# Optimization experiments

Hardware: AMD Instinct MI355X
Metric: run time of the kernel (lower is better)

The kernel has to match this reference:

```python
import jax, jax.numpy as jnp
import numpy as np

NUM_USERS = 100000
NUM_ITEMS = 100000
EMB_DIM = 64
NUM_NODES = NUM_USERS + NUM_ITEMS
NUM_EDGES = 4000000
BATCH = 4096
NUM_LAYERS = 2


def setup_inputs() -> dict:
    key = jax.random.key(0)
    ks = jax.random.split(key, 8)
    user = jax.random.randint(ks[0], (BATCH,), 0, NUM_USERS, dtype=jnp.int64) if jax.config.jax_enable_x64 else jax.random.randint(ks[0], (BATCH,), 0, NUM_USERS, dtype=jnp.int32)
    pos = jax.random.randint(ks[1], (BATCH,), 0, NUM_ITEMS, dtype=jnp.int32)
    neg = jax.random.randint(ks[2], (BATCH,), 0, NUM_ITEMS, dtype=jnp.int32)
    edge_row = jax.random.randint(ks[3], (NUM_EDGES,), 0, NUM_NODES, dtype=jnp.int32)
    edge_col = jax.random.randint(ks[4], (NUM_EDGES,), 0, NUM_NODES, dtype=jnp.int32)
    # normalized adjacency values (degree-normalized in real LightGCN)
    edge_val = jax.random.uniform(ks[5], (NUM_EDGES,), dtype=jnp.float32) * 0.01
    user_emb = jax.random.normal(ks[6], (NUM_USERS, EMB_DIM), dtype=jnp.float32) * 0.01
    item_emb = jax.random.normal(ks[7], (NUM_ITEMS, EMB_DIM), dtype=jnp.float32) * 0.01
    return {"user": user, "pos": pos, "neg": neg,
            "edge_row": edge_row, "edge_col": edge_col, "edge_val": edge_val,
            "user_emb": user_emb, "item_emb": item_emb}


def _spmm(edge_row, edge_col, edge_val, x):
    # out[r] = sum_e val[e] * x[col[e]]  -- sparse adjacency times dense emb
    msgs = edge_val[:, None] * x[edge_col]  # [E, D]
    return jax.ops.segment_sum(msgs, edge_row, num_segments=NUM_NODES)


def reference(user, pos, neg, edge_row, edge_col, edge_val, user_emb, item_emb):
    all_emb = jnp.concatenate([user_emb, item_emb], axis=0)  # [N, D]
    acc = all_emb
    h = all_emb
    for _ in range(NUM_LAYERS):
        h = _spmm(edge_row, edge_col, edge_val, h)
        acc = acc + h
    lightgcn_out = acc / (NUM_LAYERS + 1)  # mean over stacked layer embeddings
    u = lightgcn_out[:NUM_USERS]
    i = lightgcn_out[NUM_USERS:]
    user_latent = u[user]          # [B, D]
    positive_latent = i[pos]       # [B, D]
    negative_latent = i[neg]       # [B, D]
    positive_score = jnp.sum(user_latent * positive_latent, axis=1)
    negative_score = jnp.sum(user_latent * negative_latent, axis=1)
    return positive_score, negative_score
```

## Files before the change

### kernel.cpp

```cpp
#include <hip/hip_runtime.h>
#include <cstdint>
#include <cstddef>

#define NUM_USERS 100000
#define NUM_ITEMS 100000
#define NUM_NODES 200000
#define NUM_EDGES 4000000
#define BATCH     4096
#define EMB       64

#define NB    391
#define CAP   11264
#define CHUNK 8192
#define PTHREADS 1024
#define EPB   8
#define RPT   11
#define NWORDS 6250


__device__ __forceinline__ unsigned short f2bf(float f) {
    unsigned u = __float_as_uint(f);
    u = (u + 0x7FFFu + ((u >> 16) & 1u)) >> 16;
    return (unsigned short)u;
}
__device__ __forceinline__ float bf2f(unsigned short b) {
    return __uint_as_float(((unsigned)b) << 16);
}


__global__ void k_part1(const int* __restrict__ user, const int* __restrict__ pos,
                        const int* __restrict__ neg,
                        const int* __restrict__ erow, const int* __restrict__ ecol,
                        const float* __restrict__ eval_,
                        const float* __restrict__ uemb, const float* __restrict__ iemb,
                        unsigned short* __restrict__ xb,
                        int* __restrict__ bcur,
                        unsigned* __restrict__ memb, unsigned* __restrict__ need,
                        int2* __restrict__ tmp) {
    __shared__ int  hist[NB];
    __shared__ int  sst[512];
    __shared__ int  gb[NB];
    __shared__ int2 srec[CHUNK];
    int t = threadIdx.x;
    int gid = blockIdx.x * PTHREADS + t;
    if (t < NB) hist[t] = 0;

    const int TOT8 = (NUM_NODES * EMB) / 8;
    const size_t UELEMS = (size_t)NUM_USERS * EMB;
    for (int i = gid; i < TOT8; i += gridDim.x * PTHREADS) {
        size_t off = (size_t)i * 8;
        const float* src = (off < UELEMS) ? (uemb + off) : (iemb + (off - UELEMS));
        float4 f0 = ((const float4*)src)[0];
        float4 f1 = ((const float4*)src)[1];
        ((ushort4*)(xb + off))[0] = make_ushort4(f2bf(f0.x), f2bf(f0.y), f2bf(f0.z), f2bf(f0.w));
        ((ushort4*)(xb + off))[1] = make_ushort4(f2bf(f1.x), f2bf(f1.y), f2bf(f1.z), f2bf(f1.w));
    }
    if (gid < 3 * BATCH) {
        int b = gid & (BATCH - 1);
        int w = gid >> 12;
        int node = (w == 0) ? user[b] : (w == 1) ? (NUM_USERS + pos[b]) : (NUM_USERS + neg[b]);
        unsigned bit = 1u << (node & 31);
        atomicOr(&memb[node >> 5], bit);
        atomicOr(&need[node >> 5], bit);
    }
    __syncthreads();

    int start = blockIdx.x * CHUNK;
    int rows[EPB], ranks[EPB];
#pragma unroll
    for (int k = 0; k < EPB; ++k) {
        int e = start + t + k * PTHREADS;
        if (e < NUM_EDGES) {
            int r = erow[e];
            rows[k]  = r;
            ranks[k] = atomicAdd(&hist[r >> 9], 1);
        } else {
            rows[k] = -1;
        }
    }
    __syncthreads();

    if (t < 512) sst[t] = (t < NB) ? hist[t] : 0;
    __syncthreads();
    for (int off = 1; off < 512; off <<= 1) {
        int add = 0;
        if (t < 512 && t >= off) add = sst[t - off];
        __syncthreads();
        if (t < 512 && t >= off) sst[t] += add;
        __syncthreads();
    }
    if (t < NB) gb[t] = atomicAdd(&bcur[t], hist[t]);

#pragma unroll
    for (int k = 0; k < EPB; ++k) {
        if (rows[k] >= 0) {
            int e   = start + t + k * PTHREADS;
            int r   = rows[k];
            int bkt = r >> 9;
            int lp  = sst[bkt] - hist[bkt] + ranks[k];
            srec[lp] = make_int2(((r & 511) << 18) | ecol[e], __float_as_int(eval_[e]));
        }
    }
    __syncthreads();

    int wv = t >> 6, ln = t & 63;
    for (int bkt = wv; bkt < NB; bkt += 16) {
        int c  = hist[bkt];
        int st = sst[bkt] - c;
        int g0 = gb[bkt];
        size_t base = (size_t)bkt * CAP;
        for (int j = ln; j < c; j += 64) {
            int rel = g0 + j;
            if (rel < CAP)
                tmp[base + rel] = srec[st + j];
        }
    }
}


__global__ void k_part2(const int* __restrict__ bcur, const int2* __restrict__ tmp,
                        const unsigned* __restrict__ memb,
                        int2* __restrict__ epack, int2* __restrict__ rowext,
                        unsigned* __restrict__ need) {
    __shared__ int cnt[512];
    __shared__ int sc[512];
    __shared__ int loc[512];
    __shared__ unsigned mw[16];
    int b = blockIdx.x, t = threadIdx.x;
    int base_row = b << 9;
    int nrows = min(512, NUM_NODES - base_row);
    int s0 = b * CAP;
    int n = min(bcur[b], CAP);
    if (t < 512) cnt[t] = 0;
    if (t < 16) {
        int wi = (base_row >> 5) + t;
        mw[t] = (wi < NWORDS) ? memb[wi] : 0u;
    }
    __syncthreads();
    int2 r[RPT];
#pragma unroll
    for (int i = 0; i < RPT; ++i) {
        int idx = t + i * 1024;
        if (idx < n) {
            r[i] = tmp[s0 + idx];
            atomicAdd(&cnt[((unsigned)r[i].x) >> 18], 1);
        }
    }
    __syncthreads();
    int v = 0;
    if (t < 512) { v = cnt[t]; sc[t] = v; }
    __syncthreads();
    for (int off = 1; off < 512; off <<= 1) {
        int add = 0;
        if (t < 512 && t >= off) add = sc[t - off];
        __syncthreads();
        if (t < 512 && t >= off) sc[t] += add;
        __syncthreads();
    }
    if (t < 512) {
        int cur = s0 + sc[t] - v;
        if (t < nrows) rowext[base_row + t] = make_int2(cur, v);
        loc[t] = cur;
    }
    __syncthreads();
#pragma unroll
    for (int i = 0; i < RPT; ++i) {
        int idx = t + i * 1024;
        if (idx < n) {
            int2 rec = r[i];
            unsigned rl = ((unsigned)rec.x) >> 18;
            int p = atomicAdd(&loc[rl], 1);
            int col = rec.x & 0x3FFFF;
            epack[p] = make_int2(col, rec.y);
            if ((mw[rl >> 5] >> (rl & 31)) & 1u)
                atomicOr(&need[col >> 5], 1u << (col & 31));
        }
    }
}


__global__ void k_spmm1(const int2* __restrict__ rowext, const int2* __restrict__ epack,
                        const unsigned short* __restrict__ xb,
                        const unsigned* __restrict__ need,
                        unsigned short* __restrict__ h1) {
    int wid  = (blockIdx.x * blockDim.x + threadIdx.x) >> 6;
    int lane = threadIdx.x & 63;
    if (wid >= NUM_NODES) return;
    if (!((need[wid >> 5] >> (wid & 31)) & 1u)) return;
    int g = lane >> 4;
    int q = (lane & 15) * 4;
    int2 se = rowext[wid];
    int s = se.x, t = se.x + se.y;
    float a0 = 0.f, a1 = 0.f, a2 = 0.f, a3 = 0.f;
    int e = s;
    int tfull = s + ((t - s) & ~7);
    for (; e < tfull; e += 8) {
        int2 pA = epack[e + g];
        int2 pB = epack[e + 4 + g];
        float vA = __int_as_float(pA.y);
        float vB = __int_as_float(pB.y);
        ushort4 xA = *(const ushort4*)(xb + (size_t)pA.x * EMB + q);
        ushort4 xB = *(const ushort4*)(xb + (size_t)pB.x * EMB + q);
        a0 = fmaf(vA, bf2f(xA.x), a0); a1 = fmaf(vA, bf2f(xA.y), a1);
        a2 = fmaf(vA, bf2f(xA.z), a2); a3 = fmaf(vA, bf2f(xA.w), a3);
        a0 = fmaf(vB, bf2f(xB.x), a0); a1 = fmaf(vB, bf2f(xB.y), a1);
        a2 = fmaf(vB, bf2f(xB.z), a2); a3 = fmaf(vB, bf2f(xB.w), a3);
    }
    if (e < t) {
        int eA = e + g, eB = e + 4 + g;
        int2 pA = epack[eA < t ? eA : s];
        int2 pB = epack[eB < t ? eB : s];
        float vA = (eA < t) ? __int_as_float(pA.y) : 0.f;
        float vB = (eB < t) ? __int_as_float(pB.y) : 0.f;
        ushort4 xA = *(const ushort4*)(xb + (size_t)pA.x * EMB + q);
        ushort4 xB = *(const ushort4*)(xb + (size_t)pB.x * EMB + q);
        a0 = fmaf(vA, bf2f(xA.x), a0); a1 = fmaf(vA, bf2f(xA.y), a1);
        a2 = fmaf(vA, bf2f(xA.z), a2); a3 = fmaf(vA, bf2f(xA.w), a3);
        a0 = fmaf(vB, bf2f(xB.x), a0); a1 = fmaf(vB, bf2f(xB.y), a1);
        a2 = fmaf(vB, bf2f(xB.z), a2); a3 = fmaf(vB, bf2f(xB.w), a3);
    }
    a0 += __shfl_xor(a0, 16, 64); a1 += __shfl_xor(a1, 16, 64);
    a2 += __shfl_xor(a2, 16, 64); a3 += __shfl_xor(a3, 16, 64);
    a0 += __shfl_xor(a0, 32, 64); a1 += __shfl_xor(a1, 32, 64);
    a2 += __shfl_xor(a2, 32, 64); a3 += __shfl_xor(a3, 32, 64);
    if (lane < 16) {
        ushort4 o = make_ushort4(f2bf(a0), f2bf(a1), f2bf(a2), f2bf(a3));
        *(ushort4*)(h1 + (size_t)wid * EMB + q) = o;
    }
}


__device__ __forceinline__ const float* node_ptr(int c, const float* __restrict__ uemb,
                                                 const float* __restrict__ iemb) {
    return (c < NUM_USERS) ? (uemb + (size_t)c * EMB)
                           : (iemb + (size_t)(c - NUM_USERS) * EMB);
}

__global__ void k_final(const int* __restrict__ user, const int* __restrict__ pos,
                        const int* __restrict__ neg,
                        const int2* __restrict__ rowext, const int2* __restrict__ epack,
                        const float* __restrict__ uemb, const float* __restrict__ iemb,
                        const unsigned short* __restrict__ h1, float* __restrict__ out) {
    __shared__ float lds[3 * EMB];
    int b    = blockIdx.x;
    int w    = threadIdx.x >> 6;
    int lane = threadIdx.x & 63;
    int g = lane >> 4;
    int q = (lane & 15) * 4;

    int node;
    if (w == 0)      node = user[b];
    else if (w == 1) node = NUM_USERS + pos[b];
    else             node = NUM_USERS + neg[b];

    int2 se = rowext[node];
    int s = se.x, t = se.x + se.y;
    float a0 = 0.f, a1 = 0.f, a2 = 0.f, a3 = 0.f;
    for (int e = s; e < t; e += 8) {
        int eA = e + g, eB = e + 4 + g;
        int2 pA = epack[eA < t ? eA : s];
        int2 pB = epack[eB < t ? eB : s];
        float vA = (eA < t) ? __int_as_float(pA.y) : 0.f;
        float vB = (eB < t) ? __int_as_float(pB.y) : 0.f;
        ushort4 yA = *(const ushort4*)(h1 + (size_t)pA.x * EMB + q);
        ushort4 yB = *(const ushort4*)(h1 + (size_t)pB.x * EMB + q);
        a0 = fmaf(vA, bf2f(yA.x), a0); a1 = fmaf(vA, bf2f(yA.y), a1);
        a2 = fmaf(vA, bf2f(yA.z), a2); a3 = fmaf(vA, bf2f(yA.w), a3);
        a0 = fmaf(vB, bf2f(yB.x), a0); a1 = fmaf(vB, bf2f(yB.y), a1);
        a2 = fmaf(vB, bf2f(yB.z), a2); a3 = fmaf(vB, bf2f(yB.w), a3);
    }
    a0 += __shfl_xor(a0, 16, 64); a1 += __shfl_xor(a1, 16, 64);
    a2 += __shfl_xor(a2, 16, 64); a3 += __shfl_xor(a3, 16, 64);
    a0 += __shfl_xor(a0, 32, 64); a1 += __shfl_xor(a1, 32, 64);
    a2 += __shfl_xor(a2, 32, 64); a3 += __shfl_xor(a3, 32, 64);

    if (lane < 16) {
        const float* xbp = node_ptr(node, uemb, iemb) + q;
        float4  xd = *(const float4*)xbp;
        ushort4 hn = *(const ushort4*)(h1 + (size_t)node * EMB + q);
        a0 = (a0 + xd.x + bf2f(hn.x)) / 3.0f;
        a1 = (a1 + xd.y + bf2f(hn.y)) / 3.0f;
        a2 = (a2 + xd.z + bf2f(hn.z)) / 3.0f;
        a3 = (a3 + xd.w + bf2f(hn.w)) / 3.0f;
        *(float4*)(lds + w * EMB + q) = make_float4(a0, a1, a2, a3);
    }
    __syncthreads();

    if (w < 2) {
        float prod = lds[lane] * lds[(w + 1) * EMB + lane];
        for (int off = 32; off; off >>= 1) prod += __shfl_xor(prod, off, 64);
        if (lane == 0) out[w * BATCH + b] = prod;
    }
}


extern "C" void kernel_launch(void* const* d_in, const int* in_sizes, int n_in,
                              void* d_out, int out_size, void* d_ws, size_t ws_size,
                              hipStream_t stream) {
    const int*   user  = (const int*)d_in[0];
    const int*   pos   = (const int*)d_in[1];
    const int*   neg   = (const int*)d_in[2];
    const int*   erow  = (const int*)d_in[3];
    const int*   ecol  = (const int*)d_in[4];
    const float* eval_ = (const float*)d_in[5];
    const float* uemb  = (const float*)d_in[6];
    const float* iemb  = (const float*)d_in[7];
    float* out = (float*)d_out;

    char* ws = (char*)d_ws;
    unsigned short* xb = (unsigned short*)(ws);
    unsigned short* h1 = (unsigned short*)(ws + 25600000);
    int2* tmp      = (int2*)(ws + 25600000);
    int2* rowext   = (int2*)(ws + 60833792);
    int*  bcur     = (int*)(ws + 62433792);
    unsigned* memb = (unsigned*)(ws + 62435360);
    unsigned* need = (unsigned*)(ws + 62460360);
    int2* epack    = (int2*)(ws + 62485360);

    hipMemsetAsync(ws + 62433792, 0, 51568, stream);

    k_part1<<<(NUM_EDGES + CHUNK - 1) / CHUNK, PTHREADS, 0, stream>>>(
        user, pos, neg, erow, ecol, eval_, uemb, iemb, xb, bcur, memb, need, tmp);

    k_part2<<<NB, 1024, 0, stream>>>(bcur, tmp, memb, epack, rowext, need);

    k_spmm1<<<(NUM_NODES * 64 + 255) / 256, 256, 0, stream>>>(rowext, epack, xb, need, h1);

    k_final<<<BATCH, 192, 0, stream>>>(user, pos, neg, rowext, epack,
                                       uemb, iemb, h1, out);
}
```

Measured before the change: 294.6 us.

## Build per-batch-node edge lists in partition pass and sort CSR in place

```diff
diff --git a/kernel.cpp b/kernel.cpp
--- a/kernel.cpp
+++ b/kernel.cpp
@@ -15,6 +15,7 @@
 #define PTHREADS 1024
 #define EPB   8
 #define RPT   11
+#define BCAP  64
 #define NWORDS 6250
 
 
@@ -28,14 +29,30 @@
 }
 
 
-__global__ void k_part1(const int* __restrict__ user, const int* __restrict__ pos,
-                        const int* __restrict__ neg,
-                        const int* __restrict__ erow, const int* __restrict__ ecol,
+__global__ void k_mark(const int* __restrict__ user, const int* __restrict__ pos,
+                       const int* __restrict__ neg,
+                       unsigned* __restrict__ memb, unsigned* __restrict__ need,
+                       int* __restrict__ midx) {
+    int gid = blockIdx.x * blockDim.x + threadIdx.x;
+    if (gid >= 3 * BATCH) return;
+    int b = gid & (BATCH - 1);
+    int w = gid >> 12;
+    int node = (w == 0) ? user[b] : (w == 1) ? (NUM_USERS + pos[b]) : (NUM_USERS + neg[b]);
+    unsigned bit = 1u << (node & 31);
+    atomicOr(&memb[node >> 5], bit);
+    atomicOr(&need[node >> 5], bit);
+    midx[node] = gid;
+}
+
+
+__global__ void k_part1(const int* __restrict__ erow, const int* __restrict__ ecol,
                         const float* __restrict__ eval_,
                         const float* __restrict__ uemb, const float* __restrict__ iemb,
                         unsigned short* __restrict__ xb,
                         int* __restrict__ bcur,
-                        unsigned* __restrict__ memb, unsigned* __restrict__ need,
+                        const unsigned* __restrict__ memb, const int* __restrict__ midx,
+                        unsigned* __restrict__ need,
+                        int* __restrict__ bcnt, int2* __restrict__ bedge,
                         int2* __restrict__ tmp) {
     __shared__ int  hist[NB];
     __shared__ int  sst[512];
@@ -54,14 +71,6 @@
         float4 f1 = ((const float4*)src)[1];
         ((ushort4*)(xb + off))[0] = make_ushort4(f2bf(f0.x), f2bf(f0.y), f2bf(f0.z), f2bf(f0.w));
         ((ushort4*)(xb + off))[1] = make_ushort4(f2bf(f1.x), f2bf(f1.y), f2bf(f1.z), f2bf(f1.w));
-    }
-    if (gid < 3 * BATCH) {
-        int b = gid & (BATCH - 1);
-        int w = gid >> 12;
-        int node = (w == 0) ? user[b] : (w == 1) ? (NUM_USERS + pos[b]) : (NUM_USERS + neg[b]);
-        unsigned bit = 1u << (node & 31);
-        atomicOr(&memb[node >> 5], bit);
-        atomicOr(&need[node >> 5], bit);
     }
     __syncthreads();
 
@@ -96,9 +105,17 @@
         if (rows[k] >= 0) {
             int e   = start + t + k * PTHREADS;
             int r   = rows[k];
+            int c   = ecol[e];
+            int vb  = __float_as_int(eval_[e]);
             int bkt = r >> 9;
             int lp  = sst[bkt] - hist[bkt] + ranks[k];
-            srec[lp] = make_int2(((r & 511) << 18) | ecol[e], __float_as_int(eval_[e]));
+            srec[lp] = make_int2(((r & 511) << 18) | c, vb);
+            if ((memb[r >> 5] >> (r & 31)) & 1u) {
+                int cs = midx[r];
+                int p  = atomicAdd(&bcnt[cs], 1);
+                if (p < BCAP) bedge[cs * BCAP + p] = make_int2(c, vb);
+                atomicOr(&need[c >> 5], 1u << (c & 31));
+            }
         }
     }
     __syncthreads();
@@ -118,24 +135,17 @@
 }
 
 
-__global__ void k_part2(const int* __restrict__ bcur, const int2* __restrict__ tmp,
-                        const unsigned* __restrict__ memb,
-                        int2* __restrict__ epack, int2* __restrict__ rowext,
-                        unsigned* __restrict__ need) {
+__global__ void k_part2(const int* __restrict__ bcur, int2* tmp,
+                        int2* __restrict__ rowext) {
     __shared__ int cnt[512];
     __shared__ int sc[512];
     __shared__ int loc[512];
-    __shared__ unsigned mw[16];
     int b = blockIdx.x, t = threadIdx.x;
     int base_row = b << 9;
     int nrows = min(512, NUM_NODES - base_row);
     int s0 = b * CAP;
     int n = min(bcur[b], CAP);
     if (t < 512) cnt[t] = 0;
-    if (t < 16) {
-        int wi = (base_row >> 5) + t;
-        mw[t] = (wi < NWORDS) ? memb[wi] : 0u;
-    }
     __syncthreads();
     int2 r[RPT];
 #pragma unroll
@@ -170,10 +180,7 @@
             int2 rec = r[i];
             unsigned rl = ((unsigned)rec.x) >> 18;
             int p = atomicAdd(&loc[rl], 1);
-            int col = rec.x & 0x3FFFF;
-            epack[p] = make_int2(col, rec.y);
-            if ((mw[rl >> 5] >> (rl & 31)) & 1u)
-                atomicOr(&need[col >> 5], 1u << (col & 31));
+            tmp[p] = make_int2(rec.x & 0x3FFFF, rec.y);
         }
     }
 }
@@ -193,20 +200,30 @@
     int s = se.x, t = se.x + se.y;
     float a0 = 0.f, a1 = 0.f, a2 = 0.f, a3 = 0.f;
     int e = s;
-    int tfull = s + ((t - s) & ~7);
-    for (; e < tfull; e += 8) {
-        int2 pA = epack[e + g];
-        int2 pB = epack[e + 4 + g];
-        float vA = __int_as_float(pA.y);
-        float vB = __int_as_float(pB.y);
-        ushort4 xA = *(const ushort4*)(xb + (size_t)pA.x * EMB + q);
-        ushort4 xB = *(const ushort4*)(xb + (size_t)pB.x * EMB + q);
-        a0 = fmaf(vA, bf2f(xA.x), a0); a1 = fmaf(vA, bf2f(xA.y), a1);
-        a2 = fmaf(vA, bf2f(xA.z), a2); a3 = fmaf(vA, bf2f(xA.w), a3);
-        a0 = fmaf(vB, bf2f(xB.x), a0); a1 = fmaf(vB, bf2f(xB.y), a1);
-        a2 = fmaf(vB, bf2f(xB.z), a2); a3 = fmaf(vB, bf2f(xB.w), a3);
-    }
-    if (e < t) {
+    int tfull = s + ((t - s) & ~15);
+    for (; e < tfull; e += 16) {
+        int2 p0 = epack[e + g];
+        int2 p1 = epack[e + 4 + g];
+        int2 p2 = epack[e + 8 + g];
+        int2 p3 = epack[e + 12 + g];
+        ushort4 x0 = *(const ushort4*)(xb + (size_t)p0.x * EMB + q);
+        ushort4 x1 = *(const ushort4*)(xb + (size_t)p1.x * EMB + q);
+        ushort4 x2 = *(const ushort4*)(xb + (size_t)p2.x * EMB + q);
+        ushort4 x3 = *(const ushort4*)(xb + (size_t)p3.x * EMB + q);
+        float v0 = __int_as_float(p0.y);
+        float v1 = __int_as_float(p1.y);
+        float v2 = __int_as_float(p2.y);
+        float v3 = __int_as_float(p3.y);
+        a0 = fmaf(v0, bf2f(x0.x), a0); a1 = fmaf(v0, bf2f(x0.y), a1);
+        a2 = fmaf(v0, bf2f(x0.z), a2); a3 = fmaf(v0, bf2f(x0.w), a3);
+        a0 = fmaf(v1, bf2f(x1.x), a0); a1 = fmaf(v1, bf2f(x1.y), a1);
+        a2 = fmaf(v1, bf2f(x1.z), a2); a3 = fmaf(v1, bf2f(x1.w), a3);
+        a0 = fmaf(v2, bf2f(x2.x), a0); a1 = fmaf(v2, bf2f(x2.y), a1);
+        a2 = fmaf(v2, bf2f(x2.z), a2); a3 = fmaf(v2, bf2f(x2.w), a3);
+        a0 = fmaf(v3, bf2f(x3.x), a0); a1 = fmaf(v3, bf2f(x3.y), a1);
+        a2 = fmaf(v3, bf2f(x3.z), a2); a3 = fmaf(v3, bf2f(x3.w), a3);
+    }
+    for (; e < t; e += 8) {
         int eA = e + g, eB = e + 4 + g;
         int2 pA = epack[eA < t ? eA : s];
         int2 pB = epack[eB < t ? eB : s];
@@ -238,7 +255,8 @@
 
 __global__ void k_final(const int* __restrict__ user, const int* __restrict__ pos,
                         const int* __restrict__ neg,
-                        const int2* __restrict__ rowext, const int2* __restrict__ epack,
+                        const int* __restrict__ midx, const int* __restrict__ bcnt,
+                        const int2* __restrict__ bedge,
                         const float* __restrict__ uemb, const float* __restrict__ iemb,
                         const unsigned short* __restrict__ h1, float* __restrict__ out) {
     __shared__ float lds[3 * EMB];
@@ -253,13 +271,14 @@
     else if (w == 1) node = NUM_USERS + pos[b];
     else             node = NUM_USERS + neg[b];
 
-    int2 se = rowext[node];
-    int s = se.x, t = se.x + se.y;
+    int cs  = midx[node];
+    int cnt = min(bcnt[cs], BCAP);
+    int s = cs * BCAP, t = s + cnt;
     float a0 = 0.f, a1 = 0.f, a2 = 0.f, a3 = 0.f;
     for (int e = s; e < t; e += 8) {
         int eA = e + g, eB = e + 4 + g;
-        int2 pA = epack[eA < t ? eA : s];
-        int2 pB = epack[eB < t ? eB : s];
+        int2 pA = bedge[eA < t ? eA : s];
+        int2 pB = bedge[eB < t ? eB : s];
         float vA = (eA < t) ? __int_as_float(pA.y) : 0.f;
         float vB = (eB < t) ? __int_as_float(pB.y) : 0.f;
         ushort4 yA = *(const ushort4*)(h1 + (size_t)pA.x * EMB + q);
@@ -310,22 +329,26 @@
     char* ws = (char*)d_ws;
     unsigned short* xb = (unsigned short*)(ws);
     unsigned short* h1 = (unsigned short*)(ws + 25600000);
-    int2* tmp      = (int2*)(ws + 25600000);
-    int2* rowext   = (int2*)(ws + 60833792);
-    int*  bcur     = (int*)(ws + 62433792);
-    unsigned* memb = (unsigned*)(ws + 62435360);
-    unsigned* need = (unsigned*)(ws + 62460360);
-    int2* epack    = (int2*)(ws + 62485360);
-
-    hipMemsetAsync(ws + 62433792, 0, 51568, stream);
+    int2* tmp      = (int2*)(ws + 51200000);
+    int2* rowext   = (int2*)(ws + 86433792);
+    int*  bcur     = (int*)(ws + 88033792);
+    unsigned* memb = (unsigned*)(ws + 88035360);
+    unsigned* need = (unsigned*)(ws + 88060360);
+    int*  bcnt     = (int*)(ws + 88085384);
+    int*  midx     = (int*)(ws + 88134536);
+    int2* bedge    = (int2*)(ws + 88934536);
+
+    hipMemsetAsync(ws + 88033792, 0, 100744, stream);
+
+    k_mark<<<(3 * BATCH + 255) / 256, 256, 0, stream>>>(user, pos, neg, memb, need, midx);
 
     k_part1<<<(NUM_EDGES + CHUNK - 1) / CHUNK, PTHREADS, 0, stream>>>(
-        user, pos, neg, erow, ecol, eval_, uemb, iemb, xb, bcur, memb, need, tmp);
-
-    k_part2<<<NB, 1024, 0, stream>>>(bcur, tmp, memb, epack, rowext, need);
-
-    k_spmm1<<<(NUM_NODES * 64 + 255) / 256, 256, 0, stream>>>(rowext, epack, xb, need, h1);
-
-    k_final<<<BATCH, 192, 0, stream>>>(user, pos, neg, rowext, epack,
+        erow, ecol, eval_, uemb, iemb, xb, bcur, memb, midx, need, bcnt, bedge, tmp);
+
+    k_part2<<<NB, 1024, 0, stream>>>(bcur, tmp, rowext);
+
+    k_spmm1<<<(NUM_NODES * 64 + 255) / 256, 256, 0, stream>>>(rowext, tmp, xb, need, h1);
+
+    k_final<<<BATCH, 192, 0, stream>>>(user, pos, neg, midx, bcnt, bedge,
                                        uemb, iemb, h1, out);
 }
```

Measured after the change: 380.9 us. 29.3% more time.
